# Kernel optimization log

Hardware: AMD Instinct MI355X
Metric: run time of the kernel (lower is better)

## Reference

```python
import jax, jax.numpy as jnp
import numpy as np
import math

B, L, E, H, K = 4, 1024, 1024, 16, 64
D = E // H  # head_dim = 64; rel_pe has 2K+1 = 129 rows


def setup_inputs() -> dict:
    key = jax.random.key(0)
    ks = jax.random.split(key, 4)
    s = 1.0 / math.sqrt(E)
    return {
        "q": jax.random.normal(ks[0], (B, L, E), dtype=jnp.float32),
        "in_proj_weight": jax.random.normal(ks[1], (3 * E, E), dtype=jnp.float32) * s,
        "in_proj_bias": jnp.zeros((3 * E,), dtype=jnp.float32),
        "out_w": jax.random.normal(ks[2], (E, E), dtype=jnp.float32) * s,
        "out_b": jnp.zeros((E,), dtype=jnp.float32),
        "rel_pe": jax.random.normal(ks[3], (2 * K + 1, D), dtype=jnp.float32) * (1.0 / math.sqrt(D)),
    }


def _attend(q, in_proj_weight, in_proj_bias, out_w, out_b, rel_pe):
    b, l, e = q.shape
    h, d = H, D
    qkv = q @ in_proj_weight.T + in_proj_bias  # (B, L, 3E)
    qh, kh, vh = jnp.split(qkv, 3, axis=-1)
    # (B, L, E) -> (B, H, L, D)
    qh = qh.reshape(b, l, h, d).transpose(0, 2, 1, 3)
    kh = kh.reshape(b, l, h, d).transpose(0, 2, 1, 3)
    vh = vh.reshape(b, l, h, d).transpose(0, 2, 1, 3)
    qh = qh / math.sqrt(d)  # scaling applies to both content and position terms
    # content scores
    scores = jnp.einsum("bhid,bhjd->bhij", qh, kh)
    # relative-position bias: a[i, j] = rel_pe[clip(j - i, -K, K) + K]
    # compute q . rel_pe once, then gather per (i, j) -- same math as the
    # original O(L^2 * D) materialized tensor, without building it.
    pos = jnp.arange(l)
    rel = jnp.clip(pos[None, :] - pos[:, None], -K, K) + K  # (L, L) int
    bias_r = jnp.einsum("bhid,rd->bhir", qh, rel_pe)  # (B, H, L, 2K+1)
    bias = jnp.take_along_axis(bias_r, jnp.broadcast_to(rel[None, None], (b, h, l, l)), axis=-1)
    attn = jax.nn.softmax(scores + bias, axis=-1)
    out = jnp.einsum("bhij,bhjd->bhid", attn, vh)  # (B, H, L, D)
    out = out.transpose(0, 2, 1, 3).reshape(b, l, e)
    return out @ out_w.T + out_b


def reference(q, in_proj_weight, in_proj_bias, out_w, out_b, rel_pe):
    return _attend(q, in_proj_weight, in_proj_bias, out_w, out_b, rel_pe)
```

## Files before the change

kernel.cpp:

```cpp
#include <hip/hip_runtime.h>
#include <math.h>

typedef _Float16 half_t;
typedef _Float16 half8 __attribute__((ext_vector_type(8)));
typedef _Float16 half4v __attribute__((ext_vector_type(4)));
typedef float float4v __attribute__((ext_vector_type(4)));
typedef float float16v __attribute__((ext_vector_type(16)));

#define AS1 __attribute__((address_space(1)))
#define AS3 __attribute__((address_space(3)))

#define MFMA16(a, b, c) __builtin_amdgcn_mfma_f32_16x16x32_f16((a), (b), (c), 0, 0, 0)
#define MFMA32(a, b, c) __builtin_amdgcn_mfma_f32_32x32x16_f16((a), (b), (c), 0, 0, 0)

__device__ __forceinline__ void gload16(const half_t* g, half_t* l) {
    __builtin_amdgcn_global_load_lds((const AS1 void*)g, (AS3 void*)l, 16, 0, 0);
}

__device__ __forceinline__ int iclamp(int v, int lo, int hi) {
    return v < lo ? lo : (v > hi ? hi : v);
}

__global__ __launch_bounds__(256) void cast_kernel(
    const float* __restrict__ q, const float* __restrict__ w_in,
    const float* __restrict__ w_out, const float* __restrict__ pe,
    half_t* __restrict__ q16, half_t* __restrict__ w16,
    half_t* __restrict__ wo16, half_t* __restrict__ pe16)
{
    const int tid = blockIdx.x * 256 + threadIdx.x;
    const int stride = gridDim.x * 256;
    for (int i = tid; i < 1048576; i += stride) {
        float4 v = ((const float4*)q)[i];
        *(half4v*)(q16 + (size_t)i * 4) =
            (half4v){(half_t)v.x, (half_t)v.y, (half_t)v.z, (half_t)v.w};
    }
    for (int i = tid; i < 786432; i += stride) {
        float4 v = ((const float4*)w_in)[i];
        *(half4v*)(w16 + (size_t)i * 4) =
            (half4v){(half_t)v.x, (half_t)v.y, (half_t)v.z, (half_t)v.w};
    }
    for (int i = tid; i < 262144; i += stride) {
        float4 v = ((const float4*)w_out)[i];
        *(half4v*)(wo16 + (size_t)i * 4) =
            (half4v){(half_t)v.x, (half_t)v.y, (half_t)v.z, (half_t)v.w};
    }
    for (int i = tid; i < 2064; i += stride) {
        float4 v = ((const float4*)pe)[i];
        *(half4v*)(pe16 + (size_t)i * 4) =
            (half4v){(half_t)v.x, (half_t)v.y, (half_t)v.z, (half_t)v.w};
    }
    for (int i = tid; i < 496; i += stride) {
        *(half4v*)(pe16 + 8256 + (size_t)i * 4) = (half4v){0, 0, 0, 0};
    }
}

__global__ __launch_bounds__(256) void qkv_gemm(
    const half_t* __restrict__ A, const half_t* __restrict__ W,
    const float* __restrict__ bias,
    half_t* __restrict__ qh, half_t* __restrict__ kh, half_t* __restrict__ vt)
{
    __shared__ half_t As[128 * 32];
    __shared__ half_t Bs[128 * 32];
    const int K = 1024;
    const int tid = threadIdx.x, lane = tid & 63, wid = tid >> 6;
    const int wm = wid & 1, wn = wid >> 1;
    const int bid = blockIdx.x;
    const int xcd = bid & 7, idx = bid >> 3;
    const int m0 = (((xcd >> 1) << 3) + (idx & 7)) * 128;
    const int n0 = (((xcd & 1) * 12) + (idx >> 3)) * 128;

    const half_t* gA[2]; const half_t* gB[2];
    half_t* lA[2]; half_t* lB[2];
    {
        const int base = wid * 128;
#pragma unroll
        for (int c = 0; c < 2; ++c) {
            int slot = base + c * 64 + lane;
            int row = slot >> 2;
            int ch = (slot & 3) ^ ((row >> 1) & 3);
            gA[c] = A + (size_t)(m0 + row) * K + ch * 8;
            gB[c] = W + (size_t)(n0 + row) * K + ch * 8;
            lA[c] = As + (base + c * 64) * 8;
            lB[c] = Bs + (base + c * 64) * 8;
        }
    }
    int aOff[4], bOff[4];
#pragma unroll
    for (int i = 0; i < 4; ++i) {
        int ra = wm * 64 + i * 16 + (lane & 15);
        aOff[i] = ra * 32 + (((lane >> 4) ^ ((ra >> 1) & 3)) * 8);
        int rb = wn * 64 + i * 16 + (lane & 15);
        bOff[i] = rb * 32 + (((lane >> 4) ^ ((rb >> 1) & 3)) * 8);
    }
    float4v acc[4][4];
#pragma unroll
    for (int i = 0; i < 4; ++i)
#pragma unroll
        for (int j = 0; j < 4; ++j) acc[i][j] = (float4v){0.f, 0.f, 0.f, 0.f};

    for (int k0 = 0; k0 < K; k0 += 32) {
        __syncthreads();
        gload16(gA[0], lA[0]); gload16(gA[1], lA[1]);
        gload16(gB[0], lB[0]); gload16(gB[1], lB[1]);
        gA[0] += 32; gA[1] += 32; gB[0] += 32; gB[1] += 32;
        __syncthreads();
        half8 af[4], bf[4];
#pragma unroll
        for (int i = 0; i < 4; ++i) af[i] = *(const half8*)(As + aOff[i]);
#pragma unroll
        for (int j = 0; j < 4; ++j) bf[j] = *(const half8*)(Bs + bOff[j]);
#pragma unroll
        for (int i = 0; i < 4; ++i)
#pragma unroll
            for (int j = 0; j < 4; ++j)
                acc[i][j] = MFMA16(af[i], bf[j], acc[i][j]);
    }

    const int part = n0 >> 10;
#pragma unroll
    for (int ni = 0; ni < 4; ++ni) {
        const int col = n0 + wn * 64 + ni * 16 + (lane & 15);
        const float bv = bias[col];
        const int hh = (col >> 6) & 15, d = col & 63;
#pragma unroll
        for (int mi = 0; mi < 4; ++mi) {
            const int r0 = m0 + wm * 64 + mi * 16 + ((lane >> 4) << 2);
            const int bb = r0 >> 10, l0 = r0 & 1023;
            if (part == 0) {
#pragma unroll
                for (int r = 0; r < 4; ++r)
                    qh[(((size_t)(bb * 16 + hh) * 1024) + l0 + r) * 64 + d] =
                        (half_t)((acc[mi][ni][r] + bv) * 0.125f);
            } else if (part == 1) {
#pragma unroll
                for (int r = 0; r < 4; ++r)
                    kh[(((size_t)(bb * 16 + hh) * 1024) + l0 + r) * 64 + d] =
                        (half_t)(acc[mi][ni][r] + bv);
            } else {
                half4v pk;
#pragma unroll
                for (int r = 0; r < 4; ++r) pk[r] = (half_t)(acc[mi][ni][r] + bv);
                *(half4v*)(vt + ((size_t)(bb * 16 + hh) * 64 + d) * 1024 + l0) = pk;
            }
        }
    }
}

__global__ __launch_bounds__(256) void out_gemm(
    const half_t* __restrict__ A, const half_t* __restrict__ W,
    const float* __restrict__ bias, float* __restrict__ C)
{
    __shared__ half_t As[128 * 32];
    __shared__ half_t Bs[64 * 32];
    const int K = 1024;
    const int tid = threadIdx.x, lane = tid & 63, wid = tid >> 6;
    const int wm = wid & 1, wn = wid >> 1;
    const int bid = blockIdx.x;
    const int xcd = bid & 7, idx = bid >> 3;
    const int m0 = ((xcd << 2) + (idx >> 4)) * 128;
    const int n0 = (idx & 15) * 64;

    const half_t* gA[2]; const half_t* gB1;
    half_t* lA[2]; half_t* lB1;
    {
        const int base = wid * 128;
#pragma unroll
        for (int c = 0; c < 2; ++c) {
            int slot = base + c * 64 + lane;
            int row = slot >> 2;
            int ch = (slot & 3) ^ ((row >> 1) & 3);
            gA[c] = A + (size_t)(m0 + row) * K + ch * 8;
            lA[c] = As + (base + c * 64) * 8;
        }
        int slotB = wid * 64 + lane;
        int rowB = slotB >> 2;
        int chB = (slotB & 3) ^ ((rowB >> 1) & 3);
        gB1 = W + (size_t)(n0 + rowB) * K + chB * 8;
        lB1 = Bs + (wid * 64) * 8;
    }
    int aOff[4], bOff[2];
#pragma unroll
    for (int i = 0; i < 4; ++i) {
        int ra = wm * 64 + i * 16 + (lane & 15);
        aOff[i] = ra * 32 + (((lane >> 4) ^ ((ra >> 1) & 3)) * 8);
    }
#pragma unroll
    for (int j = 0; j < 2; ++j) {
        int rb = wn * 32 + j * 16 + (lane & 15);
        bOff[j] = rb * 32 + (((lane >> 4) ^ ((rb >> 1) & 3)) * 8);
    }
    float4v acc[4][2];
#pragma unroll
    for (int i = 0; i < 4; ++i)
#pragma unroll
        for (int j = 0; j < 2; ++j) acc[i][j] = (float4v){0.f, 0.f, 0.f, 0.f};

    for (int k0 = 0; k0 < K; k0 += 32) {
        __syncthreads();
        gload16(gA[0], lA[0]); gload16(gA[1], lA[1]);
        gload16(gB1, lB1);
        gA[0] += 32; gA[1] += 32; gB1 += 32;
        __syncthreads();
        half8 af[4], bf[2];
#pragma unroll
        for (int i = 0; i < 4; ++i) af[i] = *(const half8*)(As + aOff[i]);
#pragma unroll
        for (int j = 0; j < 2; ++j) bf[j] = *(const half8*)(Bs + bOff[j]);
#pragma unroll
        for (int i = 0; i < 4; ++i)
#pragma unroll
            for (int j = 0; j < 2; ++j)
                acc[i][j] = MFMA16(af[i], bf[j], acc[i][j]);
    }

#pragma unroll
    for (int ni = 0; ni < 2; ++ni) {
        const int col = n0 + wn * 32 + ni * 16 + (lane & 15);
        const float bv = bias[col];
#pragma unroll
        for (int mi = 0; mi < 4; ++mi) {
            const int r0 = m0 + wm * 64 + mi * 16 + ((lane >> 4) << 2);
#pragma unroll
            for (int r = 0; r < 4; ++r)
                C[(size_t)(r0 + r) * 1024 + col] = acc[mi][ni][r] + bv;
        }
    }
}

__global__ __launch_bounds__(256) void attn_mfma(
    const half_t* __restrict__ qh, const half_t* __restrict__ kh,
    const half_t* __restrict__ vt, const half_t* __restrict__ pe,
    half_t* __restrict__ ao)
{
    __shared__ half_t KV[8192];
    __shared__ half_t Pm[4 * 2048];
    __shared__ half_t R2[4 * 32 * 172];

    const int tid = threadIdx.x, lane = tid & 63, wid = tid >> 6;
    const int hl = lane >> 5, ql = lane & 31;
    const int bid = blockIdx.x;
    const int xcd = bid & 7, idx = bid >> 3;
    const int bh = xcd + ((idx >> 3) << 3);
    const int q0 = (idx & 7) * 128;
    const int h = bh & 15, b = bh >> 4;
    const int i0w = q0 + wid * 32;
    const size_t hbase = (size_t)(b * 16 + h) * 64 * 1024;
    const half_t* Qg = qh + hbase;
    const half_t* Kg = kh + hbase;
    const half_t* Vg = vt + hbase;

    const int qrow = i0w + ql;
    half8 qb[4];
#pragma unroll
    for (int cc = 0; cc < 4; ++cc)
        qb[cc] = *(const half8*)(Qg + (size_t)qrow * 64 + cc * 16 + hl * 8);

    const half_t* gS[4]; int lOff[4]; int ginc[4];
#pragma unroll
    for (int c = 0; c < 4; ++c) {
        const int slot0 = wid * 256 + c * 64;
        const int slot = slot0 + lane;
        if (slot0 < 512) {
            int srow = slot >> 3, sch = (slot & 7) ^ (srow & 7);
            gS[c] = Kg + srow * 64 + sch * 8;
            ginc[c] = 64 * 64;
            lOff[c] = slot0 * 8;
        } else {
            int s2 = slot - 512;
            int srow = s2 >> 3, sch = (s2 & 7) ^ (srow & 7);
            gS[c] = Vg + srow * 1024 + sch * 8;
            ginc[c] = 64;
            lOff[c] = 4096 + (slot0 - 512) * 8;
        }
    }

    half_t* r2w = R2 + wid * (32 * 172);
#pragma unroll
    for (int j2 = 0; j2 < 5; ++j2) {
        float16v c;
#pragma unroll
        for (int r = 0; r < 16; ++r) c[r] = 0.f;
#pragma unroll
        for (int cc = 0; cc < 4; ++cc) {
            half8 pb = *(const half8*)(pe + (size_t)(j2 * 32 + ql) * 64 + cc * 16 + hl * 8);
            c = MFMA32(qb[cc], pb, c);
        }
        const int col = j2 * 32 + ql;
        if (col < 129) {
#pragma unroll
            for (int reg = 0; reg < 16; ++reg) {
                const int il = (reg & 3) + 8 * (reg >> 2) + 4 * hl;
                const half_t hv = (half_t)(c[reg] - 2.0f);
                if (col == 0) {
                    for (int ts = 0; ts <= il + 4; ++ts) r2w[il * 172 + ts] = hv;
                } else if (col == 128) {
                    for (int ts = il + 132; ts <= il + 139; ++ts) r2w[il * 172 + ts] = hv;
                } else {
                    r2w[il * 172 + col + 4 + il] = hv;
                }
            }
        }
    }

    int kOff[2][4], vOff[2][4], pOff[4];
#pragma unroll
    for (int t2 = 0; t2 < 2; ++t2)
#pragma unroll
        for (int cc = 0; cc < 4; ++cc) {
            int row = t2 * 32 + ql;
            int ch = (cc * 2 + hl) ^ (row & 7);
            kOff[t2][cc] = row * 64 + ch * 8;
            vOff[t2][cc] = 4096 + row * 64 + ch * 8;
        }
    const int pwSw = (ql & 7) * 8;
    const int pwBase = wid * 2048 + ql * 64;
#pragma unroll
    for (int cc = 0; cc < 4; ++cc)
        pOff[cc] = pwBase + ((cc * 16 + hl * 8) ^ pwSw);

    const int hiC = 128 + ((ql + 3) & ~3);
    const half_t* r2row = r2w + ql * 172;

    float l_r = 0.f;
    float16v oacc[2];
#pragma unroll
    for (int dt = 0; dt < 2; ++dt)
#pragma unroll
        for (int r = 0; r < 16; ++r) oacc[dt][r] = 0.f;

    for (int kt = 0; kt < 16; ++kt) {
        __syncthreads();
#pragma unroll
        for (int c = 0; c < 4; ++c) { gload16(gS[c], KV + lOff[c]); gS[c] += ginc[c]; }
        __syncthreads();

#pragma unroll
        for (int t2 = 0; t2 < 2; ++t2) {
            float16v s;
#pragma unroll
            for (int g = 0; g < 4; ++g) {
                int traw = kt * 64 + t2 * 32 + 8 * g + 4 * hl + 64 - i0w;
                int tsb = iclamp(traw, -4, hiC) + 4;
                half4v bh4 = *(const half4v*)(r2row + tsb);
#pragma unroll
                for (int r = 0; r < 4; ++r) s[4 * g + r] = (float)bh4[r];
            }
#pragma unroll
            for (int cc = 0; cc < 4; ++cc) {
                half8 kf = *(const half8*)(KV + kOff[t2][cc]);
                s = MFMA32(kf, qb[cc], s);
            }
#pragma unroll
            for (int g = 0; g < 4; ++g) {
                half4v ph;
#pragma unroll
                for (int r = 0; r < 4; ++r) {
                    float p = __expf(s[4 * g + r]);
                    l_r += p;
                    ph[r] = (half_t)p;
                }
                const int kvb = t2 * 32 + 8 * g + 4 * hl;
                *(half4v*)(Pm + pwBase + (kvb ^ pwSw)) = ph;
            }
        }

        half8 pf[4];
#pragma unroll
        for (int cc = 0; cc < 4; ++cc) pf[cc] = *(const half8*)(Pm + pOff[cc]);
#pragma unroll
        for (int dt = 0; dt < 2; ++dt)
#pragma unroll
            for (int cc = 0; cc < 4; ++cc) {
                half8 vf = *(const half8*)(KV + vOff[dt][cc]);
                oacc[dt] = MFMA32(vf, pf[cc], oacc[dt]);
            }
    }

    l_r += __shfl_xor(l_r, 32);
    const float inv = 1.0f / l_r;

    half_t* aorow = ao + ((size_t)(b * 1024 + i0w + ql)) * 1024 + h * 64;
#pragma unroll
    for (int dt = 0; dt < 2; ++dt)
#pragma unroll
        for (int g = 0; g < 4; ++g) {
            const int d0 = dt * 32 + 8 * g + 4 * hl;
            half4v oh;
#pragma unroll
            for (int r = 0; r < 4; ++r) oh[r] = (half_t)(oacc[dt][4 * g + r] * inv);
            *(half4v*)(aorow + d0) = oh;
        }
}

extern "C" void kernel_launch(void* const* d_in, const int* in_sizes, int n_in,
                              void* d_out, int out_size, void* d_ws, size_t ws_size,
                              hipStream_t stream) {
    const float* q     = (const float*)d_in[0];
    const float* w_in  = (const float*)d_in[1];
    const float* b_in  = (const float*)d_in[2];
    const float* w_out = (const float*)d_in[3];
    const float* b_out = (const float*)d_in[4];
    const float* pe    = (const float*)d_in[5];
    float* out = (float*)d_out;

    half_t* ws = (half_t*)d_ws;
    half_t* q16   = ws;
    half_t* w16   = q16 + 4194304;
    half_t* wo16  = w16 + 3145728;
    half_t* pe16  = wo16 + 1048576;
    half_t* qh16  = pe16 + 10240;
    half_t* kh16  = qh16 + 4194304;
    half_t* vt16  = kh16 + 4194304;
    half_t* ao16  = vt16 + 4194304;

    cast_kernel<<<2048, 256, 0, stream>>>(q, w_in, w_out, pe, q16, w16, wo16, pe16);
    qkv_gemm<<<768, 256, 0, stream>>>(q16, w16, b_in, qh16, kh16, vt16);
    attn_mfma<<<512, 256, 0, stream>>>(qh16, kh16, vt16, pe16, ao16);
    out_gemm<<<512, 256, 0, stream>>>(ao16, wo16, b_out, out);
}
```

Baseline: 182.3 us.

## Double-buffer attention K/V tiles, shuffle P in registers, widen QKV GEMM K-tile

The attention kernel now double-buffers K/V tiles in LDS. The next tile's async global-to-LDS load is issued before computing on the current tile, which removes one barrier per iteration and overlaps load latency with the MFMAs. The softmax probabilities are rearranged into the PV operand layout with cross-half-wave shuffles instead of an LDS write/read round trip, freeing the Pm buffer. Separately, the QKV GEMM moves from a K-tile of 32 to 64 with a new 8-chunk XOR swizzle, halving loop iterations and barriers. The cost is more LDS per block and more register pressure, which may reduce occupancy.

Result: slower. 186.3 us (+2.2%).

```diff
diff --git a/kernel.cpp b/kernel.cpp
--- a/kernel.cpp
+++ b/kernel.cpp
@@ -19,6 +19,14 @@
 
 __device__ __forceinline__ int iclamp(int v, int lo, int hi) {
     return v < lo ? lo : (v > hi ? hi : v);
+}
+
+__device__ __forceinline__ half4v shfl32_h4(half4v v) {
+    union { half4v h; int i[2]; } u;
+    u.h = v;
+    u.i[0] = __shfl_xor(u.i[0], 32);
+    u.i[1] = __shfl_xor(u.i[1], 32);
+    return u.h;
 }
 
 __global__ __launch_bounds__(256) void cast_kernel(
@@ -59,8 +67,8 @@
     const float* __restrict__ bias,
     half_t* __restrict__ qh, half_t* __restrict__ kh, half_t* __restrict__ vt)
 {
-    __shared__ half_t As[128 * 32];
-    __shared__ half_t Bs[128 * 32];
+    __shared__ half_t As[128 * 64];
+    __shared__ half_t Bs[128 * 64];
     const int K = 1024;
     const int tid = threadIdx.x, lane = tid & 63, wid = tid >> 6;
     const int wm = wid & 1, wn = wid >> 1;
@@ -69,51 +77,56 @@
     const int m0 = (((xcd >> 1) << 3) + (idx & 7)) * 128;
     const int n0 = (((xcd & 1) * 12) + (idx >> 3)) * 128;
 
-    const half_t* gA[2]; const half_t* gB[2];
-    half_t* lA[2]; half_t* lB[2];
-    {
-        const int base = wid * 128;
-#pragma unroll
-        for (int c = 0; c < 2; ++c) {
-            int slot = base + c * 64 + lane;
-            int row = slot >> 2;
-            int ch = (slot & 3) ^ ((row >> 1) & 3);
-            gA[c] = A + (size_t)(m0 + row) * K + ch * 8;
-            gB[c] = W + (size_t)(n0 + row) * K + ch * 8;
-            lA[c] = As + (base + c * 64) * 8;
-            lB[c] = Bs + (base + c * 64) * 8;
-        }
-    }
-    int aOff[4], bOff[4];
-#pragma unroll
-    for (int i = 0; i < 4; ++i) {
-        int ra = wm * 64 + i * 16 + (lane & 15);
-        aOff[i] = ra * 32 + (((lane >> 4) ^ ((ra >> 1) & 3)) * 8);
-        int rb = wn * 64 + i * 16 + (lane & 15);
-        bOff[i] = rb * 32 + (((lane >> 4) ^ ((rb >> 1) & 3)) * 8);
-    }
+    const half_t* gA[4]; const half_t* gB[4];
+    half_t* lA[4]; half_t* lB[4];
+#pragma unroll
+    for (int c = 0; c < 4; ++c) {
+        int slot0 = wid * 256 + c * 64;
+        int slot = slot0 + lane;
+        int row = slot >> 3;
+        int ch = (slot & 7) ^ (row & 7);
+        gA[c] = A + (size_t)(m0 + row) * K + ch * 8;
+        gB[c] = W + (size_t)(n0 + row) * K + ch * 8;
+        lA[c] = As + slot0 * 8;
+        lB[c] = Bs + slot0 * 8;
+    }
+    int aOff[4][2], bOff[4][2];
+#pragma unroll
+    for (int i = 0; i < 4; ++i)
+#pragma unroll
+        for (int ks = 0; ks < 2; ++ks) {
+            int ra = wm * 64 + i * 16 + (lane & 15);
+            aOff[i][ks] = ra * 64 + (((ks * 4 + (lane >> 4)) ^ (ra & 7)) * 8);
+            int rb = wn * 64 + i * 16 + (lane & 15);
+            bOff[i][ks] = rb * 64 + (((ks * 4 + (lane >> 4)) ^ (rb & 7)) * 8);
+        }
     float4v acc[4][4];
 #pragma unroll
     for (int i = 0; i < 4; ++i)
 #pragma unroll
         for (int j = 0; j < 4; ++j) acc[i][j] = (float4v){0.f, 0.f, 0.f, 0.f};
 
-    for (int k0 = 0; k0 < K; k0 += 32) {
+    for (int k0 = 0; k0 < K; k0 += 64) {
         __syncthreads();
-        gload16(gA[0], lA[0]); gload16(gA[1], lA[1]);
-        gload16(gB[0], lB[0]); gload16(gB[1], lB[1]);
-        gA[0] += 32; gA[1] += 32; gB[0] += 32; gB[1] += 32;
+#pragma unroll
+        for (int c = 0; c < 4; ++c) {
+            gload16(gA[c], lA[c]); gload16(gB[c], lB[c]);
+            gA[c] += 64; gB[c] += 64;
+        }
         __syncthreads();
-        half8 af[4], bf[4];
-#pragma unroll
-        for (int i = 0; i < 4; ++i) af[i] = *(const half8*)(As + aOff[i]);
-#pragma unroll
-        for (int j = 0; j < 4; ++j) bf[j] = *(const half8*)(Bs + bOff[j]);
-#pragma unroll
-        for (int i = 0; i < 4; ++i)
-#pragma unroll
-            for (int j = 0; j < 4; ++j)
-                acc[i][j] = MFMA16(af[i], bf[j], acc[i][j]);
+#pragma unroll
+        for (int ks = 0; ks < 2; ++ks) {
+            half8 af[4], bf[4];
+#pragma unroll
+            for (int i = 0; i < 4; ++i) af[i] = *(const half8*)(As + aOff[i][ks]);
+#pragma unroll
+            for (int j = 0; j < 4; ++j) bf[j] = *(const half8*)(Bs + bOff[j][ks]);
+#pragma unroll
+            for (int i = 0; i < 4; ++i)
+#pragma unroll
+                for (int j = 0; j < 4; ++j)
+                    acc[i][j] = MFMA16(af[i], bf[j], acc[i][j]);
+        }
     }
 
     const int part = n0 >> 10;
@@ -232,8 +245,7 @@
     const half_t* __restrict__ vt, const half_t* __restrict__ pe,
     half_t* __restrict__ ao)
 {
-    __shared__ half_t KV[8192];
-    __shared__ half_t Pm[4 * 2048];
+    __shared__ half_t KV[2 * 8192];
     __shared__ half_t R2[4 * 32 * 172];
 
     const int tid = threadIdx.x, lane = tid & 63, wid = tid >> 6;
@@ -273,6 +285,8 @@
             lOff[c] = 4096 + (slot0 - 512) * 8;
         }
     }
+#pragma unroll
+    for (int c = 0; c < 4; ++c) { gload16(gS[c], KV + lOff[c]); gS[c] += ginc[c]; }
 
     half_t* r2w = R2 + wid * (32 * 172);
 #pragma unroll
@@ -302,7 +316,7 @@
         }
     }
 
-    int kOff[2][4], vOff[2][4], pOff[4];
+    int kOff[2][4], vOff[2][4];
 #pragma unroll
     for (int t2 = 0; t2 < 2; ++t2)
 #pragma unroll
@@ -312,11 +326,6 @@
             kOff[t2][cc] = row * 64 + ch * 8;
             vOff[t2][cc] = 4096 + row * 64 + ch * 8;
         }
-    const int pwSw = (ql & 7) * 8;
-    const int pwBase = wid * 2048 + ql * 64;
-#pragma unroll
-    for (int cc = 0; cc < 4; ++cc)
-        pOff[cc] = pwBase + ((cc * 16 + hl * 8) ^ pwSw);
 
     const int hiC = 128 + ((ql + 3) & ~3);
     const half_t* r2row = r2w + ql * 172;
@@ -330,10 +339,14 @@
 
     for (int kt = 0; kt < 16; ++kt) {
         __syncthreads();
-#pragma unroll
-        for (int c = 0; c < 4; ++c) { gload16(gS[c], KV + lOff[c]); gS[c] += ginc[c]; }
-        __syncthreads();
-
+        const int cur = (kt & 1) * 8192;
+        if (kt < 15) {
+            const int nxt = ((kt + 1) & 1) * 8192;
+#pragma unroll
+            for (int c = 0; c < 4; ++c) { gload16(gS[c], KV + nxt + lOff[c]); gS[c] += ginc[c]; }
+        }
+
+        half4v P4[2][4];
 #pragma unroll
         for (int t2 = 0; t2 < 2; ++t2) {
             float16v s;
@@ -347,31 +360,43 @@
             }
 #pragma unroll
             for (int cc = 0; cc < 4; ++cc) {
-                half8 kf = *(const half8*)(KV + kOff[t2][cc]);
+                half8 kf = *(const half8*)(KV + cur + kOff[t2][cc]);
                 s = MFMA32(kf, qb[cc], s);
             }
 #pragma unroll
             for (int g = 0; g < 4; ++g) {
-                half4v ph;
 #pragma unroll
                 for (int r = 0; r < 4; ++r) {
                     float p = __expf(s[4 * g + r]);
                     l_r += p;
-                    ph[r] = (half_t)p;
+                    P4[t2][g][r] = (half_t)p;
                 }
-                const int kvb = t2 * 32 + 8 * g + 4 * hl;
-                *(half4v*)(Pm + pwBase + (kvb ^ pwSw)) = ph;
-            }
-        }
-
+            }
+        }
+
+        half4v rcv[2][2];
+#pragma unroll
+        for (int t = 0; t < 2; ++t)
+#pragma unroll
+            for (int k = 0; k < 2; ++k) {
+                half4v send = hl ? P4[t][2 * k] : P4[t][2 * k + 1];
+                rcv[t][k] = shfl32_h4(send);
+            }
         half8 pf[4];
 #pragma unroll
-        for (int cc = 0; cc < 4; ++cc) pf[cc] = *(const half8*)(Pm + pOff[cc]);
+        for (int cc = 0; cc < 4; ++cc) {
+            const int t = cc >> 1, k = cc & 1;
+            half4v lo = hl ? rcv[t][k] : P4[t][2 * k];
+            half4v hi = hl ? P4[t][2 * k + 1] : rcv[t][k];
+#pragma unroll
+            for (int r = 0; r < 4; ++r) { pf[cc][r] = lo[r]; pf[cc][4 + r] = hi[r]; }
+        }
+
 #pragma unroll
         for (int dt = 0; dt < 2; ++dt)
 #pragma unroll
             for (int cc = 0; cc < 4; ++cc) {
-                half8 vf = *(const half8*)(KV + vOff[dt][cc]);
+                half8 vf = *(const half8*)(KV + cur + vOff[dt][cc]);
                 oacc[dt] = MFMA32(vf, pf[cc], oacc[dt]);
             }
     }
```
